# Kernel optimization log

Measured on AMD Instinct MI355X. Metric: run time of the kernel, lower is better.

The kernel has to match this reference:

```python
import jax, jax.numpy as jnp
import numpy as np

N = 100000; E = 1600000; G = 256
DIMS = [16, 64, 128, 128, 64]
HEADS = 4


def _self_loops(edge_index, n):
    loop = jnp.arange(n, dtype=edge_index.dtype)
    row = jnp.concatenate([edge_index[0], loop])  # source nodes j
    col = jnp.concatenate([edge_index[1], loop])  # target nodes i (aggregation index)
    return row, col


def _gcn(x, row, col, W, b, n):
    deg = jax.ops.segment_sum(jnp.ones_like(col, jnp.float32), col, num_segments=n)
    dis = jax.lax.rsqrt(deg)  # self-loops guarantee deg >= 1
    norm = dis[row] * dis[col]  # [E+N]
    h = x @ W  # [N, dout]
    return jax.ops.segment_sum(h[row] * norm[:, None], col, num_segments=n) + b


def _gat(x, row, col, W, a_src, a_dst, b, n):
    # PyG GATConv with self-loops; per-edge softmax over incoming neighborhoods.
    H, C = a_src.shape
    h = (x @ W).reshape(n, H, C)
    asrc = jnp.einsum('nhc,hc->nh', h, a_src)
    adst = jnp.einsum('nhc,hc->nh', h, a_dst)
    e = jax.nn.leaky_relu(asrc[row] + adst[col], 0.2)  # [E+N, H]
    m = jax.ops.segment_max(e, col, num_segments=n)
    ex = jnp.exp(e - m[col])
    s = jax.ops.segment_sum(ex, col, num_segments=n)
    alpha = ex / s[col]  # segment softmax over edges sharing a target
    out = jax.ops.segment_sum(h[row] * alpha[..., None], col, num_segments=n)
    return out.reshape(n, H * C) + b  # heads concatenated so residual add is valid


def _bn(x, g, b):
    # BatchNorm1d training-mode normalization (biased variance), eps=1e-5
    mu = jnp.mean(x, 0)
    var = jnp.var(x, 0)
    return (x - mu) * jax.lax.rsqrt(var + 1e-5) * g + b


def _forward(x, edge_index, batch, p):
    row, col = _self_loops(edge_index, N)
    gat_at = {0: 0, 2: 1}  # layers 0 and 2 have attention (i % 2 == 0 and i < n-1)
    n_layers = len(DIMS) - 1
    for i in range(n_layers):
        x = _gcn(x, row, col, p['gcn_w'][i], p['gcn_b'][i], N)
        x = _bn(x, p['bn_g'][i], p['bn_b'][i])
        if i in gat_at:
            j = gat_at[i]
            x = _gat(x, row, col, p['gat_w'][j], p['gat_asrc'][j], p['gat_adst'][j], p['gat_b'][j], N) + x
        if i < n_layers - 1:
            x = jax.nn.leaky_relu(x, 0.2)
            # dropout: identity in eval mode
    sums = jax.ops.segment_sum(x, batch, num_segments=G)
    cnt = jax.ops.segment_sum(jnp.ones((N,), jnp.float32), batch, num_segments=G)
    return sums / jnp.maximum(cnt, 1.0)[:, None]  # global_mean_pool -> [G, latent]


def setup_inputs() -> dict:
    key = jax.random.key(0)
    ks = jax.random.split(key, 16)
    inp = {}
    inp['x'] = jax.random.normal(ks[0], (N, DIMS[0]), jnp.float32)
    inp['edge_index'] = jax.random.randint(ks[1], (2, E), 0, N, dtype=jnp.int32)
    inp['batch'] = jnp.sort(jax.random.randint(ks[2], (N,), 0, G, dtype=jnp.int32))
    k = 3
    for i in range(4):
        din, dout = DIMS[i], DIMS[i + 1]
        inp[f'gcn_w{i}'] = jax.random.normal(ks[k], (din, dout), jnp.float32) / np.sqrt(din).astype(np.float32); k += 1
        inp[f'gcn_b{i}'] = jnp.zeros((dout,), jnp.float32)
        inp[f'bn_g{i}'] = jnp.ones((dout,), jnp.float32)
        inp[f'bn_b{i}'] = jnp.zeros((dout,), jnp.float32)
    for i in (0, 2):
        d = DIMS[i + 1]; C = d // HEADS
        inp[f'gat_w{i}'] = jax.random.normal(ks[k], (d, d), jnp.float32) / np.sqrt(d).astype(np.float32); k += 1
        inp[f'gat_asrc{i}'] = jax.random.normal(ks[k], (HEADS, C), jnp.float32) * 0.1; k += 1
        inp[f'gat_adst{i}'] = jax.random.normal(ks[k], (HEADS, C), jnp.float32) * 0.1; k += 1
        inp[f'gat_b{i}'] = jnp.zeros((d,), jnp.float32)
    return inp


def reference(x, edge_index, batch,
              gcn_w0, gcn_b0, bn_g0, bn_b0,
              gcn_w1, gcn_b1, bn_g1, bn_b1,
              gcn_w2, gcn_b2, bn_g2, bn_b2,
              gcn_w3, gcn_b3, bn_g3, bn_b3,
              gat_w0, gat_asrc0, gat_adst0, gat_b0,
              gat_w2, gat_asrc2, gat_adst2, gat_b2):
    p = {
        'gcn_w': [gcn_w0, gcn_w1, gcn_w2, gcn_w3],
        'gcn_b': [gcn_b0, gcn_b1, gcn_b2, gcn_b3],
        'bn_g': [bn_g0, bn_g1, bn_g2, bn_g3],
        'bn_b': [bn_b0, bn_b1, bn_b2, bn_b3],
        'gat_w': [gat_w0, gat_w2],
        'gat_asrc': [gat_asrc0, gat_asrc2],
        'gat_adst': [gat_adst0, gat_adst2],
        'gat_b': [gat_b0, gat_b2],
    }
    return _forward(x, edge_index, batch, p)
```

## Files before the change

kernel.cpp:

```cpp
#include <hip/hip_runtime.h>

static constexpr int GRAPHS = 256;
static constexpr int SCAN_CHUNK = 1024;
static constexpr int XCDS = 8;
static constexpr int SREP = 8;

typedef _Float16 h16;
typedef _Float16 h16x2 __attribute__((ext_vector_type(2)));
typedef _Float16 h16x4 __attribute__((ext_vector_type(4)));
typedef _Float16 v8h __attribute__((ext_vector_type(8)));
typedef float v4f __attribute__((ext_vector_type(4)));

__device__ __forceinline__ float lrelu(float v) { return fmaxf(v, 0.2f * v); }
__device__ __forceinline__ int rfl(int v) { return __builtin_amdgcn_readfirstlane(v); }

__global__ void zero_f32_kernel(float* __restrict__ p, int n) {
  int i = blockIdx.x * blockDim.x + threadIdx.x;
  if (i < n) p[i] = 0.0f;
}

__global__ void init_counts_kernel(int* __restrict__ cnt, int n) {
  int i = blockIdx.x * blockDim.x + threadIdx.x;
  if (i < n) cnt[i] = 1;
}

__global__ void count_edges_kernel(const int* __restrict__ ei, int* __restrict__ cnt, int E,
                                   int nb) {
  int p = blockIdx.x & (XCDS - 1);
  int lo = p * nb, hi = lo + nb;
  int nchunks = gridDim.x >> 3;
  int chunk = blockIdx.x >> 3;
  int stride = nchunks * blockDim.x;
  for (int e = chunk * blockDim.x + threadIdx.x; e < E; e += stride) {
    int c = ei[E + e];
    if (c >= lo && c < hi) atomicAdd(&cnt[c], 1);
  }
}

__global__ void block_sum_kernel(const int* __restrict__ counts, int* __restrict__ partial,
                                 int n) {
  __shared__ int sh[256];
  int base = blockIdx.x * SCAN_CHUNK;
  int t = threadIdx.x;
  int lim = min(base + SCAN_CHUNK, n);
  int s = 0;
  for (int i = base + t; i < lim; i += 256) s += counts[i];
  sh[t] = s;
  __syncthreads();
  for (int off = 128; off > 0; off >>= 1) {
    if (t < off) sh[t] += sh[t + off];
    __syncthreads();
  }
  if (t == 0) partial[blockIdx.x] = sh[0];
}

__global__ void partial_scan_kernel(int* __restrict__ partial, int* __restrict__ rowptr,
                                    int nblocks, int n) {
  __shared__ int sh[256];
  int t = threadIdx.x;
  int v = (t < nblocks) ? partial[t] : 0;
  sh[t] = v;
  __syncthreads();
  for (int off = 1; off < 256; off <<= 1) {
    int u = (t >= off) ? sh[t - off] : 0;
    __syncthreads();
    sh[t] += u;
    __syncthreads();
  }
  if (t < nblocks) partial[t] = sh[t] - v;
  if (t == 255) rowptr[n] = sh[255];
}

__global__ void chunk_scan_kernel(const int* __restrict__ counts, const int* __restrict__ partial,
                                  int* __restrict__ rowptr, int n) {
  __shared__ int sh[256];
  int base = blockIdx.x * SCAN_CHUNK;
  int t = threadIdx.x;
  int i0 = base + t * 4;
  int c0 = 0, c1 = 0, c2 = 0, c3 = 0;
  if (i0 + 3 < n) {
    int4 c = *(const int4*)(counts + i0);
    c0 = c.x;
    c1 = c.y;
    c2 = c.z;
    c3 = c.w;
  } else {
    if (i0 < n) c0 = counts[i0];
    if (i0 + 1 < n) c1 = counts[i0 + 1];
    if (i0 + 2 < n) c2 = counts[i0 + 2];
  }
  int tot = c0 + c1 + c2 + c3;
  sh[t] = tot;
  __syncthreads();
  for (int off = 1; off < 256; off <<= 1) {
    int u = (t >= off) ? sh[t - off] : 0;
    __syncthreads();
    sh[t] += u;
    __syncthreads();
  }
  int run = partial[blockIdx.x] + sh[t] - tot;
  if (i0 < n) { rowptr[i0] = run; run += c0; }
  if (i0 + 1 < n) { rowptr[i0 + 1] = run; run += c1; }
  if (i0 + 2 < n) { rowptr[i0 + 2] = run; run += c2; }
  if (i0 + 3 < n) { rowptr[i0 + 3] = run; }
}

__global__ void finalize_csr_kernel(const int* __restrict__ rowptr, float* __restrict__ dis,
                                    int* __restrict__ cursor, int* __restrict__ csr, int n) {
  int i = blockIdx.x * blockDim.x + threadIdx.x;
  if (i >= n) return;
  int s = rowptr[i], e = rowptr[i + 1];
  dis[i] = rsqrtf((float)(e - s));
  csr[s] = i;
  cursor[i] = s + 1;
}

__global__ void fill_edges_kernel(const int* __restrict__ ei, int* __restrict__ cursor,
                                  int* __restrict__ csr, int E, int nb) {
  int p = blockIdx.x & (XCDS - 1);
  int lo = p * nb, hi = lo + nb;
  int nchunks = gridDim.x >> 3;
  int chunk = blockIdx.x >> 3;
  int stride = nchunks * blockDim.x;
  for (int e = chunk * blockDim.x + threadIdx.x; e < E; e += stride) {
    int c = ei[E + e];
    if (c >= lo && c < hi) {
      int pos = atomicAdd(&cursor[c], 1);
      csr[pos] = ei[e];
    }
  }
}

__global__ void wt_all_kernel(const float* __restrict__ w0, const float* __restrict__ w1,
                              const float* __restrict__ w2, const float* __restrict__ w3,
                              const float* __restrict__ w4, h16* __restrict__ t0,
                              h16* __restrict__ t1, h16* __restrict__ t2, h16* __restrict__ t3,
                              h16* __restrict__ t4) {
  int gid = blockIdx.x * blockDim.x + threadIdx.x;
  if (gid < 4096) {
    int k = gid / 64, n = gid % 64;
    t0[n * 64 + k] = (h16)w0[gid];
  } else if (gid < 12288) {
    int i = gid - 4096;
    int k = i / 128, n = i % 128;
    t1[n * 64 + k] = (h16)w1[i];
  } else if (gid < 28672) {
    int i = gid - 12288;
    int k = i / 128, n = i % 128;
    t2[n * 128 + k] = (h16)w2[i];
  } else if (gid < 45056) {
    int i = gid - 28672;
    int k = i / 128, n = i % 128;
    t3[n * 128 + k] = (h16)w3[i];
  } else if (gid < 53248) {
    int i = gid - 45056;
    int k = i / 64, n = i % 64;
    t4[n * 128 + k] = (h16)w4[i];
  }
}

template <int K, int N, bool STATS>
__global__ void gemm_mfma_kernel(const h16* __restrict__ x, const h16* __restrict__ WT,
                                 const float* __restrict__ bias, const float* __restrict__ coefIn,
                                 h16* __restrict__ out, double* __restrict__ stats, int n_nodes) {
  constexpr int KP = K + 8;
  constexpr int NT = N / 16;
  __shared__ h16 Ah[128 * KP];
  __shared__ h16 Bs[N * KP];
  __shared__ float sh1[N], sh2[N];
  int tid = threadIdx.x;
  int node0 = blockIdx.x * 128;
  int limit = min(128, n_nodes - node0);
  if (STATS && tid < N) {
    sh1[tid] = 0.f;
    sh2[tid] = 0.f;
  }
  for (int i = tid; i < 128 * (K / 8); i += 256) {
    int row = i / (K / 8), kb = i % (K / 8);
    v8h v = {};
    if (row < limit) {
      v = *(const v8h*)(x + (size_t)(node0 + row) * K + kb * 8);
      if (coefIn) {
#pragma unroll
        for (int j = 0; j < 8; ++j)
          v[j] = (h16)fmaf((float)v[j], coefIn[kb * 8 + j], coefIn[K + kb * 8 + j]);
      }
    }
    *(v8h*)(Ah + row * KP + kb * 8) = v;
  }
  for (int i = tid; i < N * (K / 8); i += 256) {
    int nrow = i / (K / 8), kb = i % (K / 8);
    *(v8h*)(Bs + nrow * KP + kb * 8) = *(const v8h*)(WT + (size_t)nrow * K + kb * 8);
  }
  __syncthreads();

  int w = tid >> 6, lane = tid & 63, quad = lane >> 4, l16 = lane & 15;
  v4f acc[2][NT];
#pragma unroll
  for (int rt = 0; rt < 2; ++rt)
#pragma unroll
    for (int nt = 0; nt < NT; ++nt) acc[rt][nt] = (v4f){0.f, 0.f, 0.f, 0.f};

  int rowb = w * 32;
#pragma unroll
  for (int ks = 0; ks < K / 32; ++ks) {
    v8h a0 = *(const v8h*)(Ah + (rowb + l16) * KP + ks * 32 + quad * 8);
    v8h a1 = *(const v8h*)(Ah + (rowb + 16 + l16) * KP + ks * 32 + quad * 8);
#pragma unroll
    for (int nt = 0; nt < NT; ++nt) {
      v8h b = *(const v8h*)(Bs + (nt * 16 + l16) * KP + ks * 32 + quad * 8);
      acc[0][nt] = __builtin_amdgcn_mfma_f32_16x16x32_f16(a0, b, acc[0][nt], 0, 0, 0);
      acc[1][nt] = __builtin_amdgcn_mfma_f32_16x16x32_f16(a1, b, acc[1][nt], 0, 0, 0);
    }
  }

#pragma unroll
  for (int nt = 0; nt < NT; ++nt) {
    int col = nt * 16 + l16;
    float bv = bias ? bias[col] : 0.f;
    float p1 = 0.f, p2 = 0.f;
#pragma unroll
    for (int rt = 0; rt < 2; ++rt) {
#pragma unroll
      for (int reg = 0; reg < 4; ++reg) {
        int row = rowb + rt * 16 + quad * 4 + reg;
        if (row < limit) {
          float v = acc[rt][nt][reg] + bv;
          out[(size_t)(node0 + row) * N + col] = (h16)v;
          if (STATS) {
            p1 += v;
            p2 = fmaf(v, v, p2);
          }
        }
      }
    }
    if (STATS) {
      atomicAdd(&sh1[col], p1);
      atomicAdd(&sh2[col], p2);
    }
  }
  if (STATS) {
    __syncthreads();
    double* st = stats + (blockIdx.x & (SREP - 1)) * 256;
    if (tid < N) {
      atomicAdd(&st[tid], (double)sh1[tid]);
      atomicAdd(&st[N + tid], (double)sh2[tid]);
    }
  }
}

template <int K, int DOUT, int MT, bool STATS>
__global__ void gemm_tile_kernel(const h16* __restrict__ x, const float* __restrict__ W,
                                 const float* __restrict__ bias, h16* __restrict__ out,
                                 double* __restrict__ stats, int n_nodes) {
  constexpr int COLG = DOUT / 4;
  constexpr int ROWG = 256 / COLG;
  constexpr int NODES = ROWG * MT;
  constexpr int KP = K + 4;
  __shared__ float xs[NODES * KP];
  __shared__ float sh1[DOUT], sh2[DOUT];
  int tid = threadIdx.x;
  if (STATS && tid < DOUT) {
    sh1[tid] = 0.f;
    sh2[tid] = 0.f;
  }
  int node0 = blockIdx.x * NODES;
  int limit = min(NODES, n_nodes - node0);
  const h16x4* src = (const h16x4*)(x + (size_t)node0 * K);
  int tile_q = (limit * K) >> 2;
  for (int i = tid; i < tile_q; i += 256) {
    h16x4 v = src[i];
    int row = i / (K / 4), cq = i % (K / 4);
    float4 f;
    f.x = (float)v[0];
    f.y = (float)v[1];
    f.z = (float)v[2];
    f.w = (float)v[3];
    *(float4*)(xs + row * KP + cq * 4) = f;
  }
  __syncthreads();
  int cg = tid % COLG, rg = tid / COLG;
  int c0 = cg * 4;
  float acc[MT][4];
#pragma unroll
  for (int m = 0; m < MT; ++m)
#pragma unroll
    for (int i = 0; i < 4; ++i) acc[m][i] = 0.f;

  for (int k4 = 0; k4 < K / 4; ++k4) {
    int k = k4 * 4;
    float4 w0 = *(const float4*)(W + (size_t)(k + 0) * DOUT + c0);
    float4 w1 = *(const float4*)(W + (size_t)(k + 1) * DOUT + c0);
    float4 w2 = *(const float4*)(W + (size_t)(k + 2) * DOUT + c0);
    float4 w3 = *(const float4*)(W + (size_t)(k + 3) * DOUT + c0);
#pragma unroll
    for (int m = 0; m < MT; ++m) {
      float4 xv = *(const float4*)(xs + (rg * MT + m) * KP + k);
      acc[m][0] = fmaf(xv.x, w0.x, acc[m][0]);
      acc[m][1] = fmaf(xv.x, w0.y, acc[m][1]);
      acc[m][2] = fmaf(xv.x, w0.z, acc[m][2]);
      acc[m][3] = fmaf(xv.x, w0.w, acc[m][3]);
      acc[m][0] = fmaf(xv.y, w1.x, acc[m][0]);
      acc[m][1] = fmaf(xv.y, w1.y, acc[m][1]);
      acc[m][2] = fmaf(xv.y, w1.z, acc[m][2]);
      acc[m][3] = fmaf(xv.y, w1.w, acc[m][3]);
      acc[m][0] = fmaf(xv.z, w2.x, acc[m][0]);
      acc[m][1] = fmaf(xv.z, w2.y, acc[m][1]);
      acc[m][2] = fmaf(xv.z, w2.z, acc[m][2]);
      acc[m][3] = fmaf(xv.z, w2.w, acc[m][3]);
      acc[m][0] = fmaf(xv.w, w3.x, acc[m][0]);
      acc[m][1] = fmaf(xv.w, w3.y, acc[m][1]);
      acc[m][2] = fmaf(xv.w, w3.z, acc[m][2]);
      acc[m][3] = fmaf(xv.w, w3.w, acc[m][3]);
    }
  }
  float4 bv = make_float4(0.f, 0.f, 0.f, 0.f);
  if (bias) bv = *(const float4*)(bias + c0);
  float p1[4] = {0.f, 0.f, 0.f, 0.f}, p2[4] = {0.f, 0.f, 0.f, 0.f};
#pragma unroll
  for (int m = 0; m < MT; ++m) {
    int node = node0 + rg * MT + m;
    if (node < n_nodes) {
      float v0 = acc[m][0] + bv.x, v1 = acc[m][1] + bv.y;
      float v2 = acc[m][2] + bv.z, v3 = acc[m][3] + bv.w;
      h16x4 r;
      r[0] = (h16)v0;
      r[1] = (h16)v1;
      r[2] = (h16)v2;
      r[3] = (h16)v3;
      *(h16x4*)(out + (size_t)node * DOUT + c0) = r;
      if (STATS) {
        p1[0] += v0;
        p1[1] += v1;
        p1[2] += v2;
        p1[3] += v3;
        p2[0] = fmaf(v0, v0, p2[0]);
        p2[1] = fmaf(v1, v1, p2[1]);
        p2[2] = fmaf(v2, v2, p2[2]);
        p2[3] = fmaf(v3, v3, p2[3]);
      }
    }
  }
  if (STATS) {
#pragma unroll
    for (int i = 0; i < 4; ++i) {
      atomicAdd(&sh1[c0 + i], p1[i]);
      atomicAdd(&sh2[c0 + i], p2[i]);
    }
    __syncthreads();
    double* st = stats + (blockIdx.x & (SREP - 1)) * 256;
    if (tid < DOUT) {
      atomicAdd(&st[tid], (double)sh1[tid]);
      atomicAdd(&st[DOUT + tid], (double)sh2[tid]);
    }
  }
}

template <int D>
__global__ void bn_stats_kernel(const h16* __restrict__ x, double* __restrict__ stats, int n) {
  int tid = threadIdx.x;
  int c = tid & (D - 1);
  const int rpb = 256 / D;
  float s1 = 0.f, s2 = 0.f;
  for (int r = blockIdx.x * rpb + tid / D; r < n; r += gridDim.x * rpb) {
    float v = (float)x[(size_t)r * D + c];
    s1 += v;
    s2 = fmaf(v, v, s2);
  }
  double* st = stats + (blockIdx.x & (SREP - 1)) * 256;
  atomicAdd(&st[c], (double)s1);
  atomicAdd(&st[D + c], (double)s2);
}

template <int D>
__global__ void bn_coef_kernel(const double* __restrict__ stats, const float* __restrict__ g,
                               const float* __restrict__ b, float* __restrict__ coef, int n) {
  int c = threadIdx.x;
  if (c >= D) return;
  double s1 = 0.0, s2 = 0.0;
#pragma unroll
  for (int r = 0; r < SREP; ++r) {
    s1 += stats[r * 256 + c];
    s2 += stats[r * 256 + D + c];
  }
  double inv_n = 1.0 / (double)n;
  double mu = s1 * inv_n;
  double var = s2 * inv_n - mu * mu;
  float A = (float)(1.0 / sqrt(var + 1e-5)) * g[c];
  coef[c] = A;
  coef[D + c] = b[c] - (float)mu * A;
}

__global__ void gcn_agg16_kernel(const float* __restrict__ h, const int* __restrict__ rowptr,
                                 const int* __restrict__ csr, const float* __restrict__ dis,
                                 h16* __restrict__ out, int n) {
  int wave = (blockIdx.x * blockDim.x + threadIdx.x) >> 6;
  int lane = threadIdx.x & 63;
  if (wave >= n) return;
  int s = rowptr[wave], e = rowptr[wave + 1];
  int q = lane >> 4, c = lane & 15;
  float acc = 0.f;
  for (int k = s + q; k < e; k += 4) {
    int j = csr[k];
    acc = fmaf(dis[j], h[(size_t)j * 16 + c], acc);
  }
  acc += __shfl_xor(acc, 16, 64);
  acc += __shfl_xor(acc, 32, 64);
  if (lane < 16) out[(size_t)wave * 16 + lane] = (h16)(dis[wave] * acc);
}

__global__ void gcn_agg64_kernel(const h16* __restrict__ h, const int* __restrict__ rowptr,
                                 const int* __restrict__ csr, const float* __restrict__ dis,
                                 const float* __restrict__ bias, h16* __restrict__ out, int n) {
  int wave = (blockIdx.x * blockDim.x + threadIdx.x) >> 6;
  int lane = threadIdx.x & 63;
  if (wave >= n) return;
  int s = rfl(rowptr[wave]);
  int e = rfl(rowptr[wave + 1]);
  float a[4] = {0.f, 0.f, 0.f, 0.f};
  int k = s;
  for (; k + 8 <= e; k += 8) {
    int j[8];
    float d[8];
#pragma unroll
    for (int u = 0; u < 8; ++u) j[u] = rfl(csr[k + u]);
#pragma unroll
    for (int u = 0; u < 8; ++u) d[u] = dis[j[u]];
#pragma unroll
    for (int u = 0; u < 8; ++u) {
      const h16* rp = h + (size_t)j[u] * 64;
      a[u & 3] = fmaf(d[u], (float)rp[lane], a[u & 3]);
    }
  }
  for (; k + 4 <= e; k += 4) {
    int j[4];
#pragma unroll
    for (int u = 0; u < 4; ++u) j[u] = rfl(csr[k + u]);
#pragma unroll
    for (int u = 0; u < 4; ++u) {
      const h16* rp = h + (size_t)j[u] * 64;
      a[u] = fmaf(dis[j[u]], (float)rp[lane], a[u]);
    }
  }
  for (; k < e; ++k) {
    int j0 = rfl(csr[k]);
    const h16* rp = h + (size_t)j0 * 64;
    a[0] = fmaf(dis[j0], (float)rp[lane], a[0]);
  }
  float b0 = bias ? bias[lane] : 0.f;
  out[(size_t)wave * 64 + lane] = (h16)fmaf(dis[wave], (a[0] + a[1]) + (a[2] + a[3]), b0);
}

template <bool COEF>
__global__ void gcn_agg128_kernel(const h16* __restrict__ h, const int* __restrict__ rowptr,
                                  const int* __restrict__ csr, const float* __restrict__ dis,
                                  const float* __restrict__ coef, h16* __restrict__ out, int n) {
  int wave = (blockIdx.x * blockDim.x + threadIdx.x) >> 6;
  int lane = threadIdx.x & 63;
  if (wave >= n) return;
  int s = rfl(rowptr[wave]);
  int e = rfl(rowptr[wave + 1]);
  int c2 = lane * 2;
  float2 A2 = make_float2(0.f, 0.f), B2 = make_float2(0.f, 0.f);
  if (COEF) {
    A2 = *(const float2*)(coef + c2);
    B2 = *(const float2*)(coef + 128 + c2);
  }
  float a0[4] = {0.f, 0.f, 0.f, 0.f};
  float a1[4] = {0.f, 0.f, 0.f, 0.f};
  int k = s;
  for (; k + 8 <= e; k += 8) {
    int j[8];
    float d[8];
#pragma unroll
    for (int u = 0; u < 8; ++u) j[u] = rfl(csr[k + u]);
#pragma unroll
    for (int u = 0; u < 8; ++u) d[u] = dis[j[u]];
#pragma unroll
    for (int u = 0; u < 8; ++u) {
      const h16* rp = h + (size_t)j[u] * 128;
      h16x2 v = *(const h16x2*)(rp + c2);
      float f0 = (float)v[0], f1 = (float)v[1];
      if (COEF) {
        f0 = lrelu(fmaf(f0, A2.x, B2.x));
        f1 = lrelu(fmaf(f1, A2.y, B2.y));
      }
      a0[u & 3] = fmaf(d[u], f0, a0[u & 3]);
      a1[u & 3] = fmaf(d[u], f1, a1[u & 3]);
    }
  }
  for (; k < e; ++k) {
    int j0 = rfl(csr[k]);
    float d0 = dis[j0];
    const h16* rp = h + (size_t)j0 * 128;
    h16x2 v = *(const h16x2*)(rp + c2);
    float f0 = (float)v[0], f1 = (float)v[1];
    if (COEF) {
      f0 = lrelu(fmaf(f0, A2.x, B2.x));
      f1 = lrelu(fmaf(f1, A2.y, B2.y));
    }
    a0[0] = fmaf(d0, f0, a0[0]);
    a1[0] = fmaf(d0, f1, a1[0]);
  }
  float di = dis[wave];
  h16x2 r;
  r[0] = (h16)(di * ((a0[0] + a0[1]) + (a0[2] + a0[3])));
  r[1] = (h16)(di * ((a1[0] + a1[1]) + (a1[2] + a1[3])));
  *(h16x2*)(out + (size_t)wave * 128 + c2) = r;
}

template <int C>
__global__ void att_coef_kernel(const h16* __restrict__ h2, const float* __restrict__ a_src,
                                const float* __restrict__ a_dst, float* __restrict__ asrc,
                                float* __restrict__ adst, int n) {
  int gid = blockIdx.x * blockDim.x + threadIdx.x;
  if (gid >= n * 4) return;
  int nd = gid >> 2, h = gid & 3;
  const h16* hr = h2 + (size_t)nd * 4 * C + h * C;
  float s1 = 0.f, s2 = 0.f;
#pragma unroll
  for (int c = 0; c < C; ++c) {
    float v = (float)hr[c];
    s1 = fmaf(v, a_src[h * C + c], s1);
    s2 = fmaf(v, a_dst[h * C + c], s2);
  }
  asrc[gid] = s1;
  adst[gid] = s2;
}

__global__ void edge_coef_kernel(const int* __restrict__ rowptr, const int* __restrict__ csr,
                                 const float* __restrict__ asrc, const float* __restrict__ adst,
                                 float* __restrict__ exbuf, float* __restrict__ dinv, int n) {
  int wave = (blockIdx.x * blockDim.x + threadIdx.x) >> 6;
  int lane = threadIdx.x & 63;
  if (wave >= n) return;
  int h = lane & 3, es = lane >> 2;
  float ad = adst[wave * 4 + h];
  int s = rowptr[wave], e = rowptr[wave + 1];
  float den = 0.f;
  for (int k = s + es; k < e; k += 16) {
    int j = csr[k];
    float v = __expf(lrelu(asrc[j * 4 + h] + ad));
    exbuf[(size_t)k * 4 + h] = v;
    den += v;
  }
  den += __shfl_xor(den, 4, 64);
  den += __shfl_xor(den, 8, 64);
  den += __shfl_xor(den, 16, 64);
  den += __shfl_xor(den, 32, 64);
  if (lane < 4) dinv[wave * 4 + h] = 1.0f / den;
}

__global__ void gat_agg64_kernel(const h16* __restrict__ h2, const int* __restrict__ rowptr,
                                 const int* __restrict__ csr, const float* __restrict__ exbuf,
                                 const float* __restrict__ dinv, const float* __restrict__ bias,
                                 const h16* __restrict__ xres, const float* __restrict__ rescoef,
                                 h16* __restrict__ out, int n) {
  int wave = (blockIdx.x * blockDim.x + threadIdx.x) >> 6;
  int lane = threadIdx.x & 63;
  if (wave >= n) return;
  int head = lane >> 4;
  int s = rfl(rowptr[wave]);
  int e = rfl(rowptr[wave + 1]);
  float a[4] = {0.f, 0.f, 0.f, 0.f};
  int k = s;
  for (; k + 8 <= e; k += 8) {
    int j[8];
    float ex[8];
#pragma unroll
    for (int u = 0; u < 8; ++u) {
      j[u] = rfl(csr[k + u]);
      ex[u] = exbuf[(size_t)(k + u) * 4 + head];
    }
#pragma unroll
    for (int u = 0; u < 8; ++u) {
      const h16* rp = h2 + (size_t)j[u] * 64;
      a[u & 3] = fmaf(ex[u], (float)rp[lane], a[u & 3]);
    }
  }
  for (; k + 4 <= e; k += 4) {
    int j[4];
    float ex[4];
#pragma unroll
    for (int u = 0; u < 4; ++u) {
      j[u] = rfl(csr[k + u]);
      ex[u] = exbuf[(size_t)(k + u) * 4 + head];
    }
#pragma unroll
    for (int u = 0; u < 4; ++u) {
      const h16* rp = h2 + (size_t)j[u] * 64;
      a[u] = fmaf(ex[u], (float)rp[lane], a[u]);
    }
  }
  for (; k < e; ++k) {
    int j0 = rfl(csr[k]);
    const h16* rp = h2 + (size_t)j0 * 64;
    a[0] = fmaf(exbuf[(size_t)k * 4 + head], (float)rp[lane], a[0]);
  }
  float dv = dinv[wave * 4 + head];
  size_t base = (size_t)wave * 64;
  float xv = fmaf((float)xres[base + lane], rescoef[lane], rescoef[64 + lane]);
  float v0 = ((a[0] + a[1]) + (a[2] + a[3])) * dv + bias[lane] + xv;
  out[base + lane] = (h16)lrelu(v0);
}

__global__ void gat_agg128_kernel(const h16* __restrict__ h2, const int* __restrict__ rowptr,
                                  const int* __restrict__ csr, const float* __restrict__ exbuf,
                                  const float* __restrict__ dinv, const float* __restrict__ bias,
                                  const h16* __restrict__ xres, const float* __restrict__ rescoef,
                                  h16* __restrict__ out, int n) {
  int wave = (blockIdx.x * blockDim.x + threadIdx.x) >> 6;
  int lane = threadIdx.x & 63;
  if (wave >= n) return;
  int head = lane >> 4;
  int c2 = lane * 2;
  int s = rfl(rowptr[wave]);
  int e = rfl(rowptr[wave + 1]);
  float a0[4] = {0.f, 0.f, 0.f, 0.f};
  float a1[4] = {0.f, 0.f, 0.f, 0.f};
  int k = s;
  for (; k + 8 <= e; k += 8) {
    int j[8];
    float ex[8];
#pragma unroll
    for (int u = 0; u < 8; ++u) {
      j[u] = rfl(csr[k + u]);
      ex[u] = exbuf[(size_t)(k + u) * 4 + head];
    }
#pragma unroll
    for (int u = 0; u < 8; ++u) {
      const h16* rp = h2 + (size_t)j[u] * 128;
      h16x2 v = *(const h16x2*)(rp + c2);
      a0[u & 3] = fmaf(ex[u], (float)v[0], a0[u & 3]);
      a1[u & 3] = fmaf(ex[u], (float)v[1], a1[u & 3]);
    }
  }
  for (; k + 4 <= e; k += 4) {
    int j[4];
    float ex[4];
#pragma unroll
    for (int u = 0; u < 4; ++u) {
      j[u] = rfl(csr[k + u]);
      ex[u] = exbuf[(size_t)(k + u) * 4 + head];
    }
#pragma unroll
    for (int u = 0; u < 4; ++u) {
      const h16* rp = h2 + (size_t)j[u] * 128;
      h16x2 v = *(const h16x2*)(rp + c2);
      a0[u] = fmaf(ex[u], (float)v[0], a0[u]);
      a1[u] = fmaf(ex[u], (float)v[1], a1[u]);
    }
  }
  for (; k < e; ++k) {
    int j0 = rfl(csr[k]);
    float e0 = exbuf[(size_t)k * 4 + head];
    const h16* rp = h2 + (size_t)j0 * 128;
    h16x2 v = *(const h16x2*)(rp + c2);
    a0[0] = fmaf(e0, (float)v[0], a0[0]);
    a1[0] = fmaf(e0, (float)v[1], a1[0]);
  }
  float dv = dinv[wave * 4 + head];
  float2 b2 = *(const float2*)(bias + c2);
  float2 A2 = *(const float2*)(rescoef + c2);
  float2 B2 = *(const float2*)(rescoef + 128 + c2);
  size_t base = (size_t)wave * 128;
  h16x2 xr = *(const h16x2*)(xres + base + c2);
  float xr0 = fmaf((float)xr[0], A2.x, B2.x);
  float xr1 = fmaf((float)xr[1], A2.y, B2.y);
  float v0 = ((a0[0] + a0[1]) + (a0[2] + a0[3])) * dv + b2.x + xr0;
  float v1 = ((a1[0] + a1[1]) + (a1[2] + a1[3])) * dv + b2.y + xr1;
  h16x2 r;
  r[0] = (h16)lrelu(v0);
  r[1] = (h16)lrelu(v1);
  *(h16x2*)(out + base + c2) = r;
}

__global__ void graph_bounds_kernel(const int* __restrict__ batch, int* __restrict__ bounds,
                                    int n) {
  int g = threadIdx.x;
  if (g >= GRAPHS) return;
  int lo = 0, hi = n;
  while (lo < hi) {
    int mid = (lo + hi) >> 1;
    if (batch[mid] < g)
      lo = mid + 1;
    else
      hi = mid;
  }
  bounds[g] = lo;
  if (g == 0) bounds[GRAPHS] = n;
}

__global__ void pool_kernel(const h16* __restrict__ x, const int* __restrict__ bounds,
                            const float* __restrict__ coef, float* __restrict__ out) {
  __shared__ float sh[4][64];
  int g = blockIdx.x;
  int lane = threadIdx.x & 63, w = threadIdx.x >> 6;
  int s = bounds[g], e = bounds[g + 1];
  float acc = 0.f;
  for (int r = s + w; r < e; r += 4) acc += (float)x[(size_t)r * 64 + lane];
  sh[w][lane] = acc;
  __syncthreads();
  if (w == 0) {
    float t = sh[0][lane] + sh[1][lane] + sh[2][lane] + sh[3][lane];
    float cntf = (float)(e - s);
    out[(g << 6) + lane] = fmaf(coef[lane], t, coef[64 + lane] * cntf) / fmaxf(cntf, 1.0f);
  }
}

extern "C" void kernel_launch(void* const* d_in, const int* in_sizes, int n_in, void* d_out,
                              int out_size, void* d_ws, size_t ws_size, hipStream_t stream) {
  const float* x_in = (const float*)d_in[0];
  const int* ei = (const int*)d_in[1];
  const int* batch = (const int*)d_in[2];
  const float* gcn_w[4] = {(const float*)d_in[3], (const float*)d_in[7], (const float*)d_in[11],
                           (const float*)d_in[15]};
  const float* gcn_b[4] = {(const float*)d_in[4], (const float*)d_in[8], (const float*)d_in[12],
                           (const float*)d_in[16]};
  const float* bn_g[4] = {(const float*)d_in[5], (const float*)d_in[9], (const float*)d_in[13],
                          (const float*)d_in[17]};
  const float* bn_b[4] = {(const float*)d_in[6], (const float*)d_in[10], (const float*)d_in[14],
                          (const float*)d_in[18]};
  const float* gat_w0 = (const float*)d_in[19];
  const float* gat_as0 = (const float*)d_in[20];
  const float* gat_ad0 = (const float*)d_in[21];
  const float* gat_b0 = (const float*)d_in[22];
  const float* gat_w2 = (const float*)d_in[23];
  const float* gat_as2 = (const float*)d_in[24];
  const float* gat_ad2 = (const float*)d_in[25];
  const float* gat_b2 = (const float*)d_in[26];

  const int N = in_sizes[2];
  const int E = in_sizes[1] / 2;

  char* wp = (char*)d_ws;
  auto alloc = [&](size_t bytes) -> void* {
    void* p = (void*)wp;
    wp += (bytes + 255) & ~(size_t)255;
    return p;
  };
  double* statsAll = (double*)alloc(4 * SREP * 256 * sizeof(double));
  float* coefAll = (float*)alloc(4 * 256 * sizeof(float));
  int* rowptr = (int*)alloc((size_t)(N + 1) * 4);
  int* cursor = (int*)alloc((size_t)N * 4);
  int* partial = (int*)alloc(256 * sizeof(int));
  int* csr = (int*)alloc((size_t)(N + E) * 4);
  float* dis = (float*)alloc((size_t)N * 4);
  h16* bufA = (h16*)alloc((size_t)N * 128 * 2);
  h16* bufB = (h16*)alloc((size_t)N * 128 * 2);
  h16* bufC = (h16*)alloc((size_t)N * 128 * 2);
  float* attS = (float*)alloc((size_t)N * 4 * 4);
  float* attD = (float*)alloc((size_t)N * 4 * 4);
  float* exbuf = (float*)alloc((size_t)(N + E) * 4 * 4);
  float* dinv = (float*)alloc((size_t)N * 4 * 4);
  int* bounds = (int*)alloc((size_t)(GRAPHS + 1) * 4);
  h16* wt0 = (h16*)alloc(64 * 64 * 2);
  h16* wt1 = (h16*)alloc(64 * 128 * 2);
  h16* wt2 = (h16*)alloc(128 * 128 * 2);
  h16* wt3 = (h16*)alloc(128 * 128 * 2);
  h16* wt4 = (h16*)alloc(128 * 64 * 2);
  if ((size_t)(wp - (char*)d_ws) > ws_size) return;

  double* stats0 = statsAll;
  double* stats1 = statsAll + SREP * 256;
  double* stats2 = statsAll + 2 * SREP * 256;
  double* stats3 = statsAll + 3 * SREP * 256;
  float* coef0 = coefAll;
  float* coef1 = coefAll + 256;
  float* coef2 = coefAll + 512;
  float* coef3 = coefAll + 768;

  const int B = 256;
  auto cd = [](int a, int b) { return (a + b - 1) / b; };
  const int scan_blocks = cd(N, SCAN_CHUNK);
  const int nbkt = cd(N, XCDS);

  zero_f32_kernel<<<cd(4 * SREP * 512, B), B, 0, stream>>>((float*)statsAll, 4 * SREP * 512);
  wt_all_kernel<<<cd(53248, B), B, 0, stream>>>(gat_w0, gcn_w[1], gcn_w[2], gat_w2, gcn_w[3], wt0,
                                                wt1, wt2, wt3, wt4);
  init_counts_kernel<<<cd(N, B), B, 0, stream>>>(cursor, N);
  count_edges_kernel<<<XCDS * 512, B, 0, stream>>>(ei, cursor, E, nbkt);
  block_sum_kernel<<<scan_blocks, B, 0, stream>>>(cursor, partial, N);
  partial_scan_kernel<<<1, B, 0, stream>>>(partial, rowptr, scan_blocks, N);
  chunk_scan_kernel<<<scan_blocks, B, 0, stream>>>(cursor, partial, rowptr, N);
  finalize_csr_kernel<<<cd(N, B), B, 0, stream>>>(rowptr, dis, cursor, csr, N);
  fill_edges_kernel<<<XCDS * 512, B, 0, stream>>>(ei, cursor, csr, E, nbkt);
  graph_bounds_kernel<<<1, 256, 0, stream>>>(batch, bounds, N);

  gcn_agg16_kernel<<<cd(N * 64, B), B, 0, stream>>>(x_in, rowptr, csr, dis, bufB, N);
  gemm_tile_kernel<16, 64, 8, true>
      <<<cd(N, 128), B, 0, stream>>>(bufB, gcn_w[0], gcn_b[0], bufC, stats0, N);
  bn_coef_kernel<64><<<1, 64, 0, stream>>>(stats0, bn_g[0], bn_b[0], coef0, N);
  gemm_mfma_kernel<64, 64, false>
      <<<cd(N, 128), B, 0, stream>>>(bufC, wt0, nullptr, coef0, bufB, nullptr, N);
  att_coef_kernel<16><<<cd(N * 4, B), B, 0, stream>>>(bufB, gat_as0, gat_ad0, attS, attD, N);
  edge_coef_kernel<<<cd(N * 64, B), B, 0, stream>>>(rowptr, csr, attS, attD, exbuf, dinv, N);
  gat_agg64_kernel<<<cd(N * 64, B), B, 0, stream>>>(bufB, rowptr, csr, exbuf, dinv, gat_b0, bufC,
                                                    coef0, bufA, N);

  gcn_agg64_kernel<<<cd(N * 64, B), B, 0, stream>>>(bufA, rowptr, csr, dis, nullptr, bufB, N);
  gemm_mfma_kernel<64, 128, true>
      <<<cd(N, 128), B, 0, stream>>>(bufB, wt1, gcn_b[1], nullptr, bufC, stats1, N);
  bn_coef_kernel<128><<<1, 128, 0, stream>>>(stats1, bn_g[1], bn_b[1], coef1, N);

  gcn_agg128_kernel<true><<<cd(N * 64, B), B, 0, stream>>>(bufC, rowptr, csr, dis, coef1, bufB, N);
  gemm_mfma_kernel<128, 128, true>
      <<<cd(N, 128), B, 0, stream>>>(bufB, wt2, gcn_b[2], nullptr, bufA, stats2, N);
  bn_coef_kernel<128><<<1, 128, 0, stream>>>(stats2, bn_g[2], bn_b[2], coef2, N);
  gemm_mfma_kernel<128, 128, false>
      <<<cd(N, 128), B, 0, stream>>>(bufA, wt3, nullptr, coef2, bufB, nullptr, N);
  att_coef_kernel<32><<<cd(N * 4, B), B, 0, stream>>>(bufB, gat_as2, gat_ad2, attS, attD, N);
  edge_coef_kernel<<<cd(N * 64, B), B, 0, stream>>>(rowptr, csr, attS, attD, exbuf, dinv, N);
  gat_agg128_kernel<<<cd(N * 64, B), B, 0, stream>>>(bufB, rowptr, csr, exbuf, dinv, gat_b2, bufA,
                                                     coef2, bufC, N);

  gemm_mfma_kernel<128, 64, false>
      <<<cd(N, 128), B, 0, stream>>>(bufC, wt4, nullptr, nullptr, bufB, nullptr, N);
  gcn_agg64_kernel<<<cd(N * 64, B), B, 0, stream>>>(bufB, rowptr, csr, dis, gcn_b[3], bufA, N);
  bn_stats_kernel<64><<<256, 256, 0, stream>>>(bufA, stats3, N);
  bn_coef_kernel<64><<<1, 64, 0, stream>>>(stats3, bn_g[3], bn_b[3], coef3, N);

  pool_kernel<<<GRAPHS, 256, 0, stream>>>(bufA, bounds, coef3, (float*)d_out);
}
```

Measured before the change: 911.0 us.

## Fold BN coef, attention coef and graph bounds kernels into consumer kernels

Removes the bn_coef, att_coef and graph_bounds launches. Each consumer block now recomputes the BatchNorm scale and shift from the double-precision stats into shared memory. The GAT attention dot products are computed in the MFMA GEMM epilogue from the accumulators using lane shuffles, and the pool kernel binary-searches its own graph bounds. This cuts launch count and one extra pass over the GAT feature matrix, at the cost of redundant per-block coefficient computation, an extra barrier, and more register pressure in the GEMM.

```diff
diff --git a/kernel.cpp b/kernel.cpp
--- a/kernel.cpp
+++ b/kernel.cpp
@@ -13,6 +13,27 @@
 
 __device__ __forceinline__ float lrelu(float v) { return fmaxf(v, 0.2f * v); }
 __device__ __forceinline__ int rfl(int v) { return __builtin_amdgcn_readfirstlane(v); }
+
+template <int D>
+__device__ __forceinline__ void coef_from_stats(const double* __restrict__ stats,
+                                                const float* __restrict__ g,
+                                                const float* __restrict__ b, float* csh, int tid,
+                                                int n) {
+  if (tid < D) {
+    double s1 = 0.0, s2 = 0.0;
+#pragma unroll
+    for (int r = 0; r < SREP; ++r) {
+      s1 += stats[r * 256 + tid];
+      s2 += stats[r * 256 + D + tid];
+    }
+    double inv_n = 1.0 / (double)n;
+    double mu = s1 * inv_n;
+    double var = s2 * inv_n - mu * mu;
+    float A = (float)(1.0 / sqrt(var + 1e-5)) * g[tid];
+    csh[tid] = A;
+    csh[D + tid] = b[tid] - (float)mu * A;
+  }
+}
 
 __global__ void zero_f32_kernel(float* __restrict__ p, int n) {
   int i = blockIdx.x * blockDim.x + threadIdx.x;
@@ -159,15 +180,21 @@
   }
 }
 
-template <int K, int N, bool STATS>
+template <int K, int N, bool STATS, bool COEFIN, bool ATT>
 __global__ void gemm_mfma_kernel(const h16* __restrict__ x, const h16* __restrict__ WT,
-                                 const float* __restrict__ bias, const float* __restrict__ coefIn,
-                                 h16* __restrict__ out, double* __restrict__ stats, int n_nodes) {
+                                 const float* __restrict__ bias,
+                                 const double* __restrict__ statsIn, const float* __restrict__ gIn,
+                                 const float* __restrict__ bIn, h16* __restrict__ out,
+                                 double* __restrict__ statsOut, const float* __restrict__ a_src,
+                                 const float* __restrict__ a_dst, float* __restrict__ asrcO,
+                                 float* __restrict__ adstO, int n_nodes) {
   constexpr int KP = K + 8;
   constexpr int NT = N / 16;
+  constexpr int C = N / 4;
   __shared__ h16 Ah[128 * KP];
   __shared__ h16 Bs[N * KP];
   __shared__ float sh1[N], sh2[N];
+  __shared__ float csh[COEFIN ? 2 * K : 1];
   int tid = threadIdx.x;
   int node0 = blockIdx.x * 128;
   int limit = min(128, n_nodes - node0);
@@ -175,15 +202,19 @@
     sh1[tid] = 0.f;
     sh2[tid] = 0.f;
   }
+  if (COEFIN) {
+    coef_from_stats<K>(statsIn, gIn, bIn, csh, tid, n_nodes);
+    __syncthreads();
+  }
   for (int i = tid; i < 128 * (K / 8); i += 256) {
     int row = i / (K / 8), kb = i % (K / 8);
     v8h v = {};
     if (row < limit) {
       v = *(const v8h*)(x + (size_t)(node0 + row) * K + kb * 8);
-      if (coefIn) {
+      if (COEFIN) {
 #pragma unroll
         for (int j = 0; j < 8; ++j)
-          v[j] = (h16)fmaf((float)v[j], coefIn[kb * 8 + j], coefIn[K + kb * 8 + j]);
+          v[j] = (h16)fmaf((float)v[j], csh[kb * 8 + j], csh[K + kb * 8 + j]);
       }
     }
     *(v8h*)(Ah + row * KP + kb * 8) = v;
@@ -239,9 +270,65 @@
       atomicAdd(&sh2[col], p2);
     }
   }
+
+  if (ATT) {
+    float wS[NT], wD[NT];
+#pragma unroll
+    for (int nt = 0; nt < NT; ++nt) {
+      int h = (C == 16) ? nt : (nt >> 1);
+      int cp = (C == 16) ? l16 : ((nt & 1) * 16 + l16);
+      wS[nt] = a_src[h * C + cp];
+      wD[nt] = a_dst[h * C + cp];
+    }
+#pragma unroll
+    for (int rt = 0; rt < 2; ++rt) {
+#pragma unroll
+      for (int reg = 0; reg < 4; ++reg) {
+        int row = rowb + rt * 16 + quad * 4 + reg;
+        float s0 = 0.f, s1a = 0.f, s2a = 0.f, s3 = 0.f;
+        float d0 = 0.f, d1 = 0.f, d2 = 0.f, d3 = 0.f;
+#pragma unroll
+        for (int nt = 0; nt < NT; ++nt) {
+          int h = (C == 16) ? nt : (nt >> 1);
+          float v = acc[rt][nt][reg];
+          if (h == 0) {
+            s0 = fmaf(v, wS[nt], s0);
+            d0 = fmaf(v, wD[nt], d0);
+          } else if (h == 1) {
+            s1a = fmaf(v, wS[nt], s1a);
+            d1 = fmaf(v, wD[nt], d1);
+          } else if (h == 2) {
+            s2a = fmaf(v, wS[nt], s2a);
+            d2 = fmaf(v, wD[nt], d2);
+          } else {
+            s3 = fmaf(v, wS[nt], s3);
+            d3 = fmaf(v, wD[nt], d3);
+          }
+        }
+#pragma unroll
+        for (int m = 1; m < 16; m <<= 1) {
+          s0 += __shfl_xor(s0, m, 64);
+          s1a += __shfl_xor(s1a, m, 64);
+          s2a += __shfl_xor(s2a, m, 64);
+          s3 += __shfl_xor(s3, m, 64);
+          d0 += __shfl_xor(d0, m, 64);
+          d1 += __shfl_xor(d1, m, 64);
+          d2 += __shfl_xor(d2, m, 64);
+          d3 += __shfl_xor(d3, m, 64);
+        }
+        if (row < limit && l16 < 4) {
+          float sv = (l16 == 0) ? s0 : (l16 == 1) ? s1a : (l16 == 2) ? s2a : s3;
+          float dv = (l16 == 0) ? d0 : (l16 == 1) ? d1 : (l16 == 2) ? d2 : d3;
+          asrcO[(node0 + row) * 4 + l16] = sv;
+          adstO[(node0 + row) * 4 + l16] = dv;
+        }
+      }
+    }
+  }
+
   if (STATS) {
     __syncthreads();
-    double* st = stats + (blockIdx.x & (SREP - 1)) * 256;
+    double* st = statsOut + (blockIdx.x & (SREP - 1)) * 256;
     if (tid < N) {
       atomicAdd(&st[tid], (double)sh1[tid]);
       atomicAdd(&st[N + tid], (double)sh2[tid]);
@@ -372,25 +459,6 @@
   atomicAdd(&st[D + c], (double)s2);
 }
 
-template <int D>
-__global__ void bn_coef_kernel(const double* __restrict__ stats, const float* __restrict__ g,
-                               const float* __restrict__ b, float* __restrict__ coef, int n) {
-  int c = threadIdx.x;
-  if (c >= D) return;
-  double s1 = 0.0, s2 = 0.0;
-#pragma unroll
-  for (int r = 0; r < SREP; ++r) {
-    s1 += stats[r * 256 + c];
-    s2 += stats[r * 256 + D + c];
-  }
-  double inv_n = 1.0 / (double)n;
-  double mu = s1 * inv_n;
-  double var = s2 * inv_n - mu * mu;
-  float A = (float)(1.0 / sqrt(var + 1e-5)) * g[c];
-  coef[c] = A;
-  coef[D + c] = b[c] - (float)mu * A;
-}
-
 __global__ void gcn_agg16_kernel(const float* __restrict__ h, const int* __restrict__ rowptr,
                                  const int* __restrict__ csr, const float* __restrict__ dis,
                                  h16* __restrict__ out, int n) {
@@ -454,17 +522,24 @@
 template <bool COEF>
 __global__ void gcn_agg128_kernel(const h16* __restrict__ h, const int* __restrict__ rowptr,
                                   const int* __restrict__ csr, const float* __restrict__ dis,
-                                  const float* __restrict__ coef, h16* __restrict__ out, int n) {
-  int wave = (blockIdx.x * blockDim.x + threadIdx.x) >> 6;
-  int lane = threadIdx.x & 63;
+                                  const double* __restrict__ statsIn, const float* __restrict__ g,
+                                  const float* __restrict__ b, h16* __restrict__ out, int n) {
+  __shared__ float csh[256];
+  int tid = threadIdx.x;
+  if (COEF) {
+    coef_from_stats<128>(statsIn, g, b, csh, tid, n);
+    __syncthreads();
+  }
+  int wave = (blockIdx.x * blockDim.x + tid) >> 6;
+  int lane = tid & 63;
   if (wave >= n) return;
   int s = rfl(rowptr[wave]);
   int e = rfl(rowptr[wave + 1]);
   int c2 = lane * 2;
   float2 A2 = make_float2(0.f, 0.f), B2 = make_float2(0.f, 0.f);
   if (COEF) {
-    A2 = *(const float2*)(coef + c2);
-    B2 = *(const float2*)(coef + 128 + c2);
+    A2 = make_float2(csh[c2], csh[c2 + 1]);
+    B2 = make_float2(csh[128 + c2], csh[128 + c2 + 1]);
   }
   float a0[4] = {0.f, 0.f, 0.f, 0.f};
   float a1[4] = {0.f, 0.f, 0.f, 0.f};
@@ -507,25 +582,6 @@
   r[0] = (h16)(di * ((a0[0] + a0[1]) + (a0[2] + a0[3])));
   r[1] = (h16)(di * ((a1[0] + a1[1]) + (a1[2] + a1[3])));
   *(h16x2*)(out + (size_t)wave * 128 + c2) = r;
-}
-
-template <int C>
-__global__ void att_coef_kernel(const h16* __restrict__ h2, const float* __restrict__ a_src,
-                                const float* __restrict__ a_dst, float* __restrict__ asrc,
-                                float* __restrict__ adst, int n) {
-  int gid = blockIdx.x * blockDim.x + threadIdx.x;
-  if (gid >= n * 4) return;
-  int nd = gid >> 2, h = gid & 3;
-  const h16* hr = h2 + (size_t)nd * 4 * C + h * C;
-  float s1 = 0.f, s2 = 0.f;
-#pragma unroll
-  for (int c = 0; c < C; ++c) {
-    float v = (float)hr[c];
-    s1 = fmaf(v, a_src[h * C + c], s1);
-    s2 = fmaf(v, a_dst[h * C + c], s2);
-  }
-  asrc[gid] = s1;
-  adst[gid] = s2;
 }
 
 __global__ void edge_coef_kernel(const int* __restrict__ rowptr, const int* __restrict__ csr,
@@ -554,10 +610,15 @@
 __global__ void gat_agg64_kernel(const h16* __restrict__ h2, const int* __restrict__ rowptr,
                                  const int* __restrict__ csr, const float* __restrict__ exbuf,
                                  const float* __restrict__ dinv, const float* __restrict__ bias,
-                                 const h16* __restrict__ xres, const float* __restrict__ rescoef,
+                                 const h16* __restrict__ xres, const double* __restrict__ statsIn,
+                                 const float* __restrict__ g, const float* __restrict__ b,
                                  h16* __restrict__ out, int n) {
-  int wave = (blockIdx.x * blockDim.x + threadIdx.x) >> 6;
-  int lane = threadIdx.x & 63;
+  __shared__ float csh[128];
+  int tid = threadIdx.x;
+  coef_from_stats<64>(statsIn, g, b, csh, tid, n);
+  __syncthreads();
+  int wave = (blockIdx.x * blockDim.x + tid) >> 6;
+  int lane = tid & 63;
   if (wave >= n) return;
   int head = lane >> 4;
   int s = rfl(rowptr[wave]);
@@ -599,7 +660,7 @@
   }
   float dv = dinv[wave * 4 + head];
   size_t base = (size_t)wave * 64;
-  float xv = fmaf((float)xres[base + lane], rescoef[lane], rescoef[64 + lane]);
+  float xv = fmaf((float)xres[base + lane], csh[lane], csh[64 + lane]);
   float v0 = ((a[0] + a[1]) + (a[2] + a[3])) * dv + bias[lane] + xv;
   out[base + lane] = (h16)lrelu(v0);
 }
@@ -607,10 +668,15 @@
 __global__ void gat_agg128_kernel(const h16* __restrict__ h2, const int* __restrict__ rowptr,
                                   const int* __restrict__ csr, const float* __restrict__ exbuf,
                                   const float* __restrict__ dinv, const float* __restrict__ bias,
-                                  const h16* __restrict__ xres, const float* __restrict__ rescoef,
+                                  const h16* __restrict__ xres, const double* __restrict__ statsIn,
+                                  const float* __restrict__ g, const float* __restrict__ b,
                                   h16* __restrict__ out, int n) {
-  int wave = (blockIdx.x * blockDim.x + threadIdx.x) >> 6;
-  int lane = threadIdx.x & 63;
+  __shared__ float csh[256];
+  int tid = threadIdx.x;
+  coef_from_stats<128>(statsIn, g, b, csh, tid, n);
+  __syncthreads();
+  int wave = (blockIdx.x * blockDim.x + tid) >> 6;
+  int lane = tid & 63;
   if (wave >= n) return;
   int head = lane >> 4;
   int c2 = lane * 2;
@@ -661,12 +727,10 @@
   }
   float dv = dinv[wave * 4 + head];
   float2 b2 = *(const float2*)(bias + c2);
-  float2 A2 = *(const float2*)(rescoef + c2);
-  float2 B2 = *(const float2*)(rescoef + 128 + c2);
   size_t base = (size_t)wave * 128;
   h16x2 xr = *(const h16x2*)(xres + base + c2);
-  float xr0 = fmaf((float)xr[0], A2.x, B2.x);
-  float xr1 = fmaf((float)xr[1], A2.y, B2.y);
+  float xr0 = fmaf((float)xr[0], csh[c2], csh[128 + c2]);
+  float xr1 = fmaf((float)xr[1], csh[c2 + 1], csh[129 + c2]);
   float v0 = ((a0[0] + a0[1]) + (a0[2] + a0[3])) * dv + b2.x + xr0;
   float v1 = ((a1[0] + a1[1]) + (a1[2] + a1[3])) * dv + b2.y + xr1;
   h16x2 r;
@@ -675,28 +739,30 @@
   *(h16x2*)(out + base + c2) = r;
 }
 
-__global__ void graph_bounds_kernel(const int* __restrict__ batch, int* __restrict__ bounds,
-                                    int n) {
-  int g = threadIdx.x;
-  if (g >= GRAPHS) return;
-  int lo = 0, hi = n;
-  while (lo < hi) {
-    int mid = (lo + hi) >> 1;
-    if (batch[mid] < g)
-      lo = mid + 1;
-    else
-      hi = mid;
-  }
-  bounds[g] = lo;
-  if (g == 0) bounds[GRAPHS] = n;
-}
-
-__global__ void pool_kernel(const h16* __restrict__ x, const int* __restrict__ bounds,
-                            const float* __restrict__ coef, float* __restrict__ out) {
+__global__ void pool_kernel(const h16* __restrict__ x, const int* __restrict__ batch,
+                            const double* __restrict__ statsIn, const float* __restrict__ g,
+                            const float* __restrict__ b, float* __restrict__ out, int n) {
   __shared__ float sh[4][64];
-  int g = blockIdx.x;
-  int lane = threadIdx.x & 63, w = threadIdx.x >> 6;
-  int s = bounds[g], e = bounds[g + 1];
+  __shared__ float csh[128];
+  __shared__ int sb[2];
+  int tid = threadIdx.x;
+  int gid = blockIdx.x;
+  coef_from_stats<64>(statsIn, g, b, csh, tid, n);
+  if (tid < 2) {
+    int key = gid + tid;
+    int lo = 0, hi = n;
+    while (lo < hi) {
+      int mid = (lo + hi) >> 1;
+      if (batch[mid] < key)
+        lo = mid + 1;
+      else
+        hi = mid;
+    }
+    sb[tid] = lo;
+  }
+  __syncthreads();
+  int s = sb[0], e = sb[1];
+  int lane = tid & 63, w = tid >> 6;
   float acc = 0.f;
   for (int r = s + w; r < e; r += 4) acc += (float)x[(size_t)r * 64 + lane];
   sh[w][lane] = acc;
@@ -704,7 +770,7 @@
   if (w == 0) {
     float t = sh[0][lane] + sh[1][lane] + sh[2][lane] + sh[3][lane];
     float cntf = (float)(e - s);
-    out[(g << 6) + lane] = fmaf(coef[lane], t, coef[64 + lane] * cntf) / fmaxf(cntf, 1.0f);
+    out[(gid << 6) + lane] = fmaf(csh[lane], t, csh[64 + lane] * cntf) / fmaxf(cntf, 1.0f);
   }
 }
 
@@ -740,7 +806,6 @@
     return p;
   };
   double* statsAll = (double*)alloc(4 * SREP * 256 * sizeof(double));
-  float* coefAll = (float*)alloc(4 * 256 * sizeof(float));
   int* rowptr = (int*)alloc((size_t)(N + 1) * 4);
   int* cursor = (int*)alloc((size_t)N * 4);
   int* partial = (int*)alloc(256 * sizeof(int));
@@ -753,7 +818,6 @@
   float* attD = (float*)alloc((size_t)N * 4 * 4);
   float* exbuf = (float*)alloc((size_t)(N + E) * 4 * 4);
   float* dinv = (float*)alloc((size_t)N * 4 * 4);
-  int* bounds = (int*)alloc((size_t)(GRAPHS + 1) * 4);
   h16* wt0 = (h16*)alloc(64 * 64 * 2);
   h16* wt1 = (h16*)alloc(64 * 128 * 2);
   h16* wt2 = (h16*)alloc(128 * 128 * 2);
@@ -765,10 +829,6 @@
   double* stats1 = statsAll + SREP * 256;
   double* stats2 = statsAll + 2 * SREP * 256;
   double* stats3 = statsAll + 3 * SREP * 256;
-  float* coef0 = coefAll;
-  float* coef1 = coefAll + 256;
-  float* coef2 = coefAll + 512;
-  float* coef3 = coefAll + 768;
 
   const int B = 256;
   auto cd = [](int a, int b) { return (a + b - 1) / b; };
@@ -785,40 +845,39 @@
   chunk_scan_kernel<<<scan_blocks, B, 0, stream>>>(cursor, partial, rowptr, N);
   finalize_csr_kernel<<<cd(N, B), B, 0, stream>>>(rowptr, dis, cursor, csr, N);
   fill_edges_kernel<<<XCDS * 512, B, 0, stream>>>(ei, cursor, csr, E, nbkt);
-  graph_bounds_kernel<<<1, 256, 0, stream>>>(batch, bounds, N);
 
   gcn_agg16_kernel<<<cd(N * 64, B), B, 0, stream>>>(x_in, rowptr, csr, dis, bufB, N);
   gemm_tile_kernel<16, 64, 8, true>
       <<<cd(N, 128), B, 0, stream>>>(bufB, gcn_w[0], gcn_b[0], bufC, stats0, N);
-  bn_coef_kernel<64><<<1, 64, 0, stream>>>(stats0, bn_g[0], bn_b[0], coef0, N);
-  gemm_mfma_kernel<64, 64, false>
-      <<<cd(N, 128), B, 0, stream>>>(bufC, wt0, nullptr, coef0, bufB, nullptr, N);
-  att_coef_kernel<16><<<cd(N * 4, B), B, 0, stream>>>(bufB, gat_as0, gat_ad0, attS, attD, N);
+  gemm_mfma_kernel<64, 64, false, true, true><<<cd(N, 128), B, 0, stream>>>(
+      bufC, wt0, nullptr, stats0, bn_g[0], bn_b[0], bufB, nullptr, gat_as0, gat_ad0, attS, attD,
+      N);
   edge_coef_kernel<<<cd(N * 64, B), B, 0, stream>>>(rowptr, csr, attS, attD, exbuf, dinv, N);
   gat_agg64_kernel<<<cd(N * 64, B), B, 0, stream>>>(bufB, rowptr, csr, exbuf, dinv, gat_b0, bufC,
-                                                    coef0, bufA, N);
+                                                    stats0, bn_g[0], bn_b[0], bufA, N);
 
   gcn_agg64_kernel<<<cd(N * 64, B), B, 0, stream>>>(bufA, rowptr, csr, dis, nullptr, bufB, N);
-  gemm_mfma_kernel<64, 128, true>
-      <<<cd(N, 128), B, 0, stream>>>(bufB, wt1, gcn_b[1], nullptr, bufC, stats1, N);
-  bn_coef_kernel<128><<<1, 128, 0, stream>>>(stats1, bn_g[1], bn_b[1], coef1, N);
-
-  gcn_agg128_kernel<true><<<cd(N * 64, B), B, 0, stream>>>(bufC, rowptr, csr, dis, coef1, bufB, N);
-  gemm_mfma_kernel<128, 128, true>
-      <<<cd(N, 128), B, 0, stream>>>(bufB, wt2, gcn_b[2], nullptr, bufA, stats2, N);
-  bn_coef_kernel<128><<<1, 128, 0, stream>>>(stats2, bn_g[2], bn_b[2], coef2, N);
-  gemm_mfma_kernel<128, 128, false>
-      <<<cd(N, 128), B, 0, stream>>>(bufA, wt3, nullptr, coef2, bufB, nullptr, N);
-  att_coef_kernel<32><<<cd(N * 4, B), B, 0, stream>>>(bufB, gat_as2, gat_ad2, attS, attD, N);
+  gemm_mfma_kernel<64, 128, true, false, false><<<cd(N, 128), B, 0, stream>>>(
+      bufB, wt1, gcn_b[1], nullptr, nullptr, nullptr, bufC, stats1, nullptr, nullptr, nullptr,
+      nullptr, N);
+
+  gcn_agg128_kernel<true>
+      <<<cd(N * 64, B), B, 0, stream>>>(bufC, rowptr, csr, dis, stats1, bn_g[1], bn_b[1], bufB, N);
+  gemm_mfma_kernel<128, 128, true, false, false><<<cd(N, 128), B, 0, stream>>>(
+      bufB, wt2, gcn_b[2], nullptr, nullptr, nullptr, bufA, stats2, nullptr, nullptr, nullptr,
+      nullptr, N);
+  gemm_mfma_kernel<128, 128, false, true, true><<<cd(N, 128), B, 0, stream>>>(
+      bufA, wt3, nullptr, stats2, bn_g[2], bn_b[2], bufB, nullptr, gat_as2, gat_ad2, attS, attD,
+      N);
   edge_coef_kernel<<<cd(N * 64, B), B, 0, stream>>>(rowptr, csr, attS, attD, exbuf, dinv, N);
   gat_agg128_kernel<<<cd(N * 64, B), B, 0, stream>>>(bufB, rowptr, csr, exbuf, dinv, gat_b2, bufA,
-                                                     coef2, bufC, N);
-
-  gemm_mfma_kernel<128, 64, false>
-      <<<cd(N, 128), B, 0, stream>>>(bufC, wt4, nullptr, nullptr, bufB, nullptr, N);
+                                                     stats2, bn_g[2], bn_b[2], bufC, N);
+
+  gemm_mfma_kernel<128, 64, false, false, false><<<cd(N, 128), B, 0, stream>>>(
+      bufC, wt4, nullptr, nullptr, nullptr, nullptr, bufB, nullptr, nullptr, nullptr, nullptr,
+      nullptr, N);
   gcn_agg64_kernel<<<cd(N * 64, B), B, 0, stream>>>(bufB, rowptr, csr, dis, gcn_b[3], bufA, N);
   bn_stats_kernel<64><<<256, 256, 0, stream>>>(bufA, stats3, N);
-  bn_coef_kernel<64><<<1, 64, 0, stream>>>(stats3, bn_g[3], bn_b[3], coef3, N);
-
-  pool_kernel<<<GRAPHS, 256, 0, stream>>>(bufA, bounds, coef3, (float*)d_out);
-}
+
+  pool_kernel<<<GRAPHS, 256, 0, stream>>>(bufA, batch, stats3, bn_g[3], bn_b[3], (float*)d_out, N);
+}
```

Result: no change. 922.5 us (+1.3%).
